# Kernel tuning notes

Hardware: AMD Instinct MI355X
Metric: run time of the kernel (lower is better)

Reference implementation:

```python
import jax, jax.numpy as jnp
import numpy as np

WS = 16        # window size
SHIFT = 8      # shift for odd blocks
DEPTH = 2      # number of stacked blocks
HEADS = 8
EPS = 1e-5


def window_partition(x, ws):
    # x: (B,H,W,C) -> (B*nw, ws*ws, C)
    B, H, W, C = x.shape
    x = x.reshape(B, H // ws, ws, W // ws, ws, C).transpose(0, 1, 3, 2, 4, 5)
    return x.reshape(-1, ws * ws, C)


def window_reverse(wins, ws, H, W):
    B = wins.shape[0] // ((H // ws) * (W // ws))
    x = wins.reshape(B, H // ws, W // ws, ws, ws, -1).transpose(0, 1, 3, 2, 4, 5)
    return x.reshape(B, H, W, -1)


def layernorm(x, g, b):
    m = jnp.mean(x, axis=-1, keepdims=True)
    v = jnp.mean(jnp.square(x - m), axis=-1, keepdims=True)
    return (x - m) * jax.lax.rsqrt(v + EPS) * g + b


def _make_rpi(ws):
    # Swin relative position index, shape (ws*ws, ws*ws), int32
    coords = np.stack(np.meshgrid(np.arange(ws), np.arange(ws), indexing='ij'))  # (2,ws,ws)
    coords = coords.reshape(2, -1)
    rel = coords[:, :, None] - coords[:, None, :]  # (2, n, n)
    rel = rel + (ws - 1)
    rpi = rel[0] * (2 * ws - 1) + rel[1]
    return jnp.asarray(rpi, dtype=jnp.int32)


def _make_attn_mask(H, W, ws, shift):
    # Swin shifted-window mask, shape (nw, n, n) with 0 / -100
    img = np.zeros((1, H, W, 1), dtype=np.float32)
    cnt = 0
    slices = (slice(0, -ws), slice(-ws, -shift), slice(-shift, None))
    for hs in slices:
        for wsl in slices:
            img[:, hs, wsl, :] = cnt
            cnt += 1
    mw = window_partition(jnp.asarray(img), ws).reshape(-1, ws * ws)  # (nw, n)
    mask = mw[:, None, :] - mw[:, :, None]
    return jnp.where(mask != 0, jnp.float32(-100.0), jnp.float32(0.0))


def setup_inputs() -> dict:
    key = jax.random.key(0)
    ks = jax.random.split(key, 8)
    B, H, W, C = 8, 64, 64, 256
    hid = 4 * C
    d = DEPTH
    s = 0.02
    inp = {
        'x':      jax.random.normal(ks[0], (B, H, W, C), jnp.float32),
        'ln1_g':  jnp.ones((d, C), jnp.float32),
        'ln1_b':  jnp.zeros((d, C), jnp.float32),
        'qkv_w':  jax.random.normal(ks[1], (d, C, 3 * C), jnp.float32) * s,
        'qkv_b':  jnp.zeros((d, 3 * C), jnp.float32),
        'rpb':    jax.random.normal(ks[2], (d, (2 * WS - 1) ** 2, HEADS), jnp.float32) * s,
        'proj_w': jax.random.normal(ks[3], (d, C, C), jnp.float32) * s,
        'proj_b': jnp.zeros((d, C), jnp.float32),
        'ln2_g':  jnp.ones((d, C), jnp.float32),
        'ln2_b':  jnp.zeros((d, C), jnp.float32),
        'fc1_w':  jax.random.normal(ks[4], (d, C, hid), jnp.float32) * s,
        'fc1_b':  jnp.zeros((d, hid), jnp.float32),
        'fc2_w':  jax.random.normal(ks[5], (d, hid, C), jnp.float32) * s,
        'fc2_b':  jnp.zeros((d, C), jnp.float32),
        'attn_mask': _make_attn_mask(H, W, WS, SHIFT),
        'rpi':    _make_rpi(WS),
    }
    return inp


def _forward(x, ln1_g, ln1_b, qkv_w, qkv_b, rpb, proj_w, proj_b,
             ln2_g, ln2_b, fc1_w, fc1_b, fc2_w, fc2_b, attn_mask, rpi):
    B, H, W, C = x.shape
    n = WS * WS
    hd = C // HEADS
    scale = jnp.float32(hd) ** -0.5
    for i in range(DEPTH):
        shift = SHIFT if (i % 2 == 1) else 0
        shortcut = x
        y = layernorm(x, ln1_g[i], ln1_b[i])
        if shift:
            y = jnp.roll(y, (-shift, -shift), axis=(1, 2))
        wins = window_partition(y, WS)                      # (b_, n, C)
        b_ = wins.shape[0]
        qkv = wins @ qkv_w[i] + qkv_b[i]
        qkv = qkv.reshape(b_, n, 3, HEADS, hd).transpose(2, 0, 3, 1, 4)
        q, k, v = qkv[0] * scale, qkv[1], qkv[2]            # (b_,h,n,hd)
        attn = jnp.einsum('bhnd,bhmd->bhnm', q, k)          # (b_,h,n,n)
        bias = rpb[i][rpi.reshape(-1)].reshape(n, n, HEADS).transpose(2, 0, 1)
        attn = attn + bias[None]
        if shift:
            nw = attn_mask.shape[0]
            attn = attn.reshape(B, nw, HEADS, n, n) + attn_mask[None, :, None]
            attn = attn.reshape(b_, HEADS, n, n)
        attn = jax.nn.softmax(attn, axis=-1)
        out = jnp.einsum('bhnm,bhmd->bhnd', attn, v)
        out = out.transpose(0, 2, 1, 3).reshape(b_, n, C)
        out = out @ proj_w[i] + proj_b[i]
        y = window_reverse(out, WS, H, W)
        if shift:
            y = jnp.roll(y, (shift, shift), axis=(1, 2))
        x = shortcut + y
        z = layernorm(x, ln2_g[i], ln2_b[i])
        z = jax.nn.gelu(z @ fc1_w[i] + fc1_b[i], approximate=False)
        z = z @ fc2_w[i] + fc2_b[i]
        x = x + z
    return x


def reference(x, ln1_g, ln1_b, qkv_w, qkv_b, rpb, proj_w, proj_b,
              ln2_g, ln2_b, fc1_w, fc1_b, fc2_w, fc2_b, attn_mask, rpi):
    return _forward(x, ln1_g, ln1_b, qkv_w, qkv_b, rpb, proj_w, proj_b,
                    ln2_g, ln2_b, fc1_w, fc1_b, fc2_w, fc2_b, attn_mask, rpi)
```

## Files before the change

### kernel.cpp

```cpp
#include <hip/hip_runtime.h>

typedef unsigned short u16;
typedef __attribute__((ext_vector_type(8))) short short8;
typedef __attribute__((ext_vector_type(4))) float f32x4;

#define GLDS16(gp, sp) __builtin_amdgcn_global_load_lds( \
    (const __attribute__((address_space(1))) void*)(gp),  \
    (__attribute__((address_space(3))) void*)(sp), 16, 0, 0)

__device__ __forceinline__ u16 f2bf(float f) {
  union { float f; unsigned u; } x; x.f = f;
  unsigned r = (x.u + 0x7fffu + ((x.u >> 16) & 1u)) >> 16;
  return (u16)r;
}
__device__ __forceinline__ float bf2f(u16 v) {
  union { unsigned u; float f; } x; x.u = ((unsigned)v) << 16; return x.f;
}

__global__ __launch_bounds__(256) void wswizB(const float* __restrict__ W,
                                              u16* __restrict__ Wf, int K, int N) {
  int tid = blockIdx.x * 256 + threadIdx.x;
  int Kt = K >> 5, Nt = N >> 4;
  int per = Nt * Kt * 64;
  if (tid >= 2 * per) return;
  int l = tid >= per;
  int rem = tid - l * per;
  int nb = rem / (Kt * 64);
  int rem2 = rem - nb * Kt * 64;
  int ks = rem2 >> 6, lane = rem2 & 63;
  int n = nb * 16 + (lane & 15);
  u16 o[8];
  #pragma unroll
  for (int e = 0; e < 8; ++e) {
    int k = ks * 32 + ((lane >> 4) << 3) + e;
    o[e] = f2bf(W[((size_t)l * K + k) * N + n]);
  }
  *(uint4*)(Wf + ((size_t)tid << 3)) = *(uint4*)o;
}

__global__ __launch_bounds__(256) void wswiz1(const float* __restrict__ W,
                                              u16* __restrict__ Wf) {
  int tid = blockIdx.x * 256 + threadIdx.x;
  int lane = tid & 63, nt = (tid >> 6) & 7, ks = (tid >> 9) & 7,
      hc = (tid >> 12) & 7, l = tid >> 15;
  int n = hc * 128 + nt * 16 + (lane & 15);
  u16 o[8];
  #pragma unroll
  for (int e = 0; e < 8; ++e) {
    int k = ks * 32 + ((lane >> 4) << 3) + e;
    o[e] = f2bf(W[((size_t)l * 256 + k) * 1024 + n]);
  }
  *(uint4*)(Wf + ((size_t)tid << 3)) = *(uint4*)o;
}

__global__ __launch_bounds__(256) void wswiz2(const float* __restrict__ W,
                                              u16* __restrict__ Wf) {
  int tid = blockIdx.x * 256 + threadIdx.x;
  int lane = tid & 63, nt = (tid >> 6) & 15, ks = (tid >> 10) & 3,
      hc = (tid >> 12) & 7, l = tid >> 15;
  int n = nt * 16 + (lane & 15);
  u16 o[8];
  #pragma unroll
  for (int e = 0; e < 8; ++e) {
    int k = hc * 128 + ks * 32 + ((lane >> 4) << 3) + e;
    o[e] = f2bf(W[((size_t)l * 1024 + k) * 256 + n]);
  }
  *(uint4*)(Wf + ((size_t)tid << 3)) = *(uint4*)o;
}

__global__ __launch_bounds__(256) void bias_gb(const float* __restrict__ rpb,
                                               const int* __restrict__ rpi,
                                               u16* __restrict__ biasb) {
  int tid = blockIdx.x * 256 + threadIdx.x;
  if (tid >= 131072) return;
  int l = tid >> 16, cid = tid & 65535;
  int lane = cid & 63, k = (cid >> 6) & 7, mslot = (cid >> 9) & 15, h = cid >> 13;
  u16 o[8];
  #pragma unroll
  for (int e = 0; e < 8; ++e) {
    int nt = 2 * k + (e >> 2), r = e & 3;
    int i = mslot * 16 + ((lane >> 4) << 2) + r;
    int j = nt * 16 + (lane & 15);
    int idx = rpi[i * 256 + j];
    o[e] = f2bf(rpb[((size_t)l * 961 + idx) * 8 + h]);
  }
  *(uint4*)(biasb + ((size_t)tid << 3)) = *(uint4*)o;
}

__global__ __launch_bounds__(256) void ln_part(const float* __restrict__ x,
                                               const float* __restrict__ g,
                                               const float* __restrict__ b,
                                               u16* __restrict__ out, int shift) {
  int wv = threadIdx.x >> 6, lane = threadIdx.x & 63;
  int wtok = blockIdx.x * 4 + wv;
  int w = wtok >> 8, t = wtok & 255;
  int bimg = w >> 4, wi = w & 15;
  int ph = (((wi >> 2) << 4) + (t >> 4) + shift) & 63;
  int pw = (((wi & 3) << 4) + (t & 15) + shift) & 63;
  const float4 v = *(const float4*)(x + ((size_t)((bimg * 64 + ph) * 64 + pw)) * 256 + lane * 4);
  float s = v.x + v.y + v.z + v.w;
  float sq = v.x * v.x + v.y * v.y + v.z * v.z + v.w * v.w;
  #pragma unroll
  for (int m = 1; m < 64; m <<= 1) { s += __shfl_xor(s, m, 64); sq += __shfl_xor(sq, m, 64); }
  float mean = s * (1.f / 256.f);
  float var = sq * (1.f / 256.f) - mean * mean;
  float rs = rsqrtf(var + 1e-5f);
  float4 gg = *(const float4*)(g + lane * 4);
  float4 bb = *(const float4*)(b + lane * 4);
  u16 o0 = f2bf((v.x - mean) * rs * gg.x + bb.x);
  u16 o1 = f2bf((v.y - mean) * rs * gg.y + bb.y);
  u16 o2 = f2bf((v.z - mean) * rs * gg.z + bb.z);
  u16 o3 = f2bf((v.w - mean) * rs * gg.w + bb.w);
  uint2 pk; pk.x = (unsigned)o0 | ((unsigned)o1 << 16); pk.y = (unsigned)o2 | ((unsigned)o3 << 16);
  *(uint2*)(out + (size_t)wtok * 256 + lane * 4) = pk;
}

struct EpiParams {
  const float* bias;
  u16* obf;
  float* of32;
  const float* resid;
  int shift;
  float qscale;
};

template <int EPI>
__global__ __launch_bounds__(512, 2) void gemm_fk(const u16* __restrict__ A,
                                                  const u16* __restrict__ Wf,
                                                  int N, EpiParams ep) {
  __shared__ u16 As[8][128][32];
  int tid = threadIdx.x;
  int n0 = blockIdx.x * 128, m0 = blockIdx.y * 128;
  int wv = tid >> 6, lane = tid & 63, quad = lane >> 4, l15 = lane & 15;
  int wm = wv & 1, wn = wv >> 1;

  #pragma unroll
  for (int i = 0; i < 8; ++i) {
    int c = i * 512 + tid;
    int kb = c >> 9, rc = c & 511;
    int row = rc >> 2, kc = (rc & 3) * 8;
    GLDS16(A + (size_t)(m0 + row) * 256 + kb * 32 + kc, &As[kb][row][kc]);
  }
  __syncthreads();

  f32x4 acc[4][2] = {};
  #pragma unroll
  for (int kb = 0; kb < 8; ++kb) {
    short8 bf[2];
    #pragma unroll
    for (int nt = 0; nt < 2; ++nt) {
      size_t ntile = (size_t)(blockIdx.x * 8 + wn * 2 + nt);
      bf[nt] = *(const short8*)(Wf + ((ntile * 8 + kb) * 64 + lane) * 8);
    }
    #pragma unroll
    for (int mt = 0; mt < 4; ++mt) {
      short8 af = *(const short8*)&As[kb][wm * 64 + mt * 16 + l15][quad * 8];
      #pragma unroll
      for (int nt = 0; nt < 2; ++nt)
        acc[mt][nt] = __builtin_amdgcn_mfma_f32_16x16x32_bf16(af, bf[nt], acc[mt][nt], 0, 0, 0);
    }
  }

  #pragma unroll
  for (int mt = 0; mt < 4; ++mt) {
    #pragma unroll
    for (int nt = 0; nt < 2; ++nt) {
      #pragma unroll
      for (int r = 0; r < 4; ++r) {
        int grow = m0 + wm * 64 + mt * 16 + quad * 4 + r;
        int gcol = n0 + wn * 32 + nt * 16 + l15;
        float v = acc[mt][nt][r] + ep.bias[gcol];
        if constexpr (EPI == 0) {
          if (gcol < 256) v *= ep.qscale;
          ep.obf[(size_t)grow * N + gcol] = f2bf(v);
        } else {
          int w_ = grow >> 8, t = grow & 255, wi = w_ & 15;
          int ph = (((wi >> 2) << 4) + (t >> 4) + ep.shift) & 63;
          int pw = (((wi & 3) << 4) + (t & 15) + ep.shift) & 63;
          size_t pix = (size_t)(((w_ >> 4) * 64 + ph) * 64 + pw);
          ep.of32[pix * 256 + gcol] = ep.resid[pix * 256 + gcol] + v;
        }
      }
    }
  }
}

__global__ __launch_bounds__(512, 4) void fused_mlp(const float* __restrict__ xin,
                                                    const float* __restrict__ g,
                                                    const float* __restrict__ b,
                                                    const u16* __restrict__ W1f,
                                                    const u16* __restrict__ W2f,
                                                    const float* __restrict__ b1p,
                                                    const float* __restrict__ b2p,
                                                    float* __restrict__ out) {
  __shared__ u16 Zs[64 * 264];
  __shared__ u16 Hs[2][64 * 136];
  int tid = threadIdx.x, wv = tid >> 6, lane = tid & 63;
  int quad = lane >> 4, l15 = lane & 15;
  int m0 = blockIdx.x * 64;

  float4 gg = *(const float4*)(g + lane * 4);
  float4 bb = *(const float4*)(b + lane * 4);
  #pragma unroll
  for (int rr = 0; rr < 8; ++rr) {
    int row = wv * 8 + rr;
    const float4 v = *(const float4*)(xin + (size_t)(m0 + row) * 256 + lane * 4);
    float s = v.x + v.y + v.z + v.w;
    float sq = v.x * v.x + v.y * v.y + v.z * v.z + v.w * v.w;
    #pragma unroll
    for (int m = 1; m < 64; m <<= 1) { s += __shfl_xor(s, m, 64); sq += __shfl_xor(sq, m, 64); }
    float mean = s * (1.f / 256.f);
    float var = sq * (1.f / 256.f) - mean * mean;
    float rs = rsqrtf(var + 1e-5f);
    u16 o0 = f2bf((v.x - mean) * rs * gg.x + bb.x);
    u16 o1 = f2bf((v.y - mean) * rs * gg.y + bb.y);
    u16 o2 = f2bf((v.z - mean) * rs * gg.z + bb.z);
    u16 o3 = f2bf((v.w - mean) * rs * gg.w + bb.w);
    uint2 pk; pk.x = (unsigned)o0 | ((unsigned)o1 << 16); pk.y = (unsigned)o2 | ((unsigned)o3 << 16);
    *(uint2*)&Zs[row * 264 + lane * 4] = pk;
  }
  __syncthreads();

  f32x4 acc2[4][2];
  #pragma unroll
  for (int nt = 0; nt < 2; ++nt) {
    float b2 = b2p[wv * 32 + nt * 16 + l15];
    #pragma unroll
    for (int mt = 0; mt < 4; ++mt)
      #pragma unroll
      for (int r = 0; r < 4; ++r) acc2[mt][nt][r] = b2;
  }

  for (int hc = 0; hc < 8; ++hc) {
    f32x4 acc1[4];
    {
      float b1 = b1p[hc * 128 + wv * 16 + l15];
      #pragma unroll
      for (int mt = 0; mt < 4; ++mt)
        #pragma unroll
        for (int r = 0; r < 4; ++r) acc1[mt][r] = b1;
    }
    #pragma unroll
    for (int ks = 0; ks < 8; ++ks) {
      short8 bf = *(const short8*)(W1f + ((((size_t)hc * 8 + ks) * 8 + wv) * 64 + lane) * 8);
      #pragma unroll
      for (int mt = 0; mt < 4; ++mt) {
        short8 af = *(const short8*)&Zs[(mt * 16 + l15) * 264 + ks * 32 + quad * 8];
        acc1[mt] = __builtin_amdgcn_mfma_f32_16x16x32_bf16(af, bf, acc1[mt], 0, 0, 0);
      }
    }
    u16* hs = &Hs[hc & 1][0];
    #pragma unroll
    for (int mt = 0; mt < 4; ++mt)
      #pragma unroll
      for (int r = 0; r < 4; ++r) {
        float v = acc1[mt][r];
        float inner = v * (1.f + 0.044715f * v * v);
        float e = __expf(-1.5957691216057308f * inner);
        float gl = v * __builtin_amdgcn_rcpf(1.f + e);
        hs[(mt * 16 + quad * 4 + r) * 136 + wv * 16 + l15] = f2bf(gl);
      }
    __syncthreads();
    #pragma unroll
    for (int ks = 0; ks < 4; ++ks) {
      short8 bf2[2];
      #pragma unroll
      for (int nt = 0; nt < 2; ++nt)
        bf2[nt] = *(const short8*)(W2f + ((((size_t)hc * 4 + ks) * 16 + wv * 2 + nt) * 64 + lane) * 8);
      #pragma unroll
      for (int mt = 0; mt < 4; ++mt) {
        short8 af2 = *(const short8*)&hs[(mt * 16 + l15) * 136 + ks * 32 + quad * 8];
        #pragma unroll
        for (int nt = 0; nt < 2; ++nt)
          acc2[mt][nt] = __builtin_amdgcn_mfma_f32_16x16x32_bf16(af2, bf2[nt], acc2[mt][nt], 0, 0, 0);
      }
    }
  }

  #pragma unroll
  for (int mt = 0; mt < 4; ++mt)
    #pragma unroll
    for (int nt = 0; nt < 2; ++nt)
      #pragma unroll
      for (int r = 0; r < 4; ++r) {
        size_t idx = (size_t)(m0 + mt * 16 + quad * 4 + r) * 256 + wv * 32 + nt * 16 + l15;
        out[idx] = xin[idx] + acc2[mt][nt][r];
      }
}

__global__ __launch_bounds__(256, 4) void attn_v3(const u16* __restrict__ qkv,
                                                  const u16* __restrict__ biasb,
                                                  int layer, u16* __restrict__ aout) {
  __shared__ u16 Klds[256 * 32];
  __shared__ u16 Vt[32 * 264];
  __shared__ u16 Plds[4][16 * 40];
  int bid = blockIdx.x;
  int lw = ((bid & 7) << 7) | (bid >> 3);
  int w = lw >> 3, h = lw & 7;
  int tid = threadIdx.x;

  {
    const uint4* kp = (const uint4*)(qkv + ((size_t)(w * 256 + tid)) * 768 + 256 + h * 32);
    uint4* kd = (uint4*)&Klds[tid * 32];
    kd[0] = kp[0]; kd[1] = kp[1]; kd[2] = kp[2]; kd[3] = kp[3];
    const uint4* vp = (const uint4*)(qkv + ((size_t)(w * 256 + tid)) * 768 + 512 + h * 32);
    u16 vt[32];
    *(uint4*)&vt[0]  = vp[0];
    *(uint4*)&vt[8]  = vp[1];
    *(uint4*)&vt[16] = vp[2];
    *(uint4*)&vt[24] = vp[3];
    #pragma unroll
    for (int d = 0; d < 32; ++d) Vt[d * 264 + tid] = vt[d];
  }
  __syncthreads();

  int wv = tid >> 6, lane = tid & 63, quad = lane >> 4, l15 = lane & 15;
  int wi = w & 15, wr = wi >> 2, wc = wi & 3;
  const bool masked = (layer != 0) && (wr == 3 || wc == 3);
  int rcj = (wc == 3) ? (l15 < 8 ? 1 : 2) : 0;

  #pragma unroll
  for (int mt = 0; mt < 4; ++mt) {
    int mslot = wv * 4 + mt;
    int m0 = mslot * 16;
    short8 aq = *(const short8*)(qkv + ((size_t)(w * 256 + m0 + l15)) * 768 + h * 32 + quad * 8);
    const u16* bmt = biasb + ((size_t)layer << 19) + ((size_t)h << 16) + (size_t)mslot * 4096;
    f32x4 c[16];
    #pragma unroll
    for (int k = 0; k < 8; ++k) {
      short8 bv = *(const short8*)(bmt + k * 512 + lane * 8);
      #pragma unroll
      for (int r = 0; r < 4; ++r) {
        c[2 * k][r]     = bf2f((u16)bv[r]);
        c[2 * k + 1][r] = bf2f((u16)bv[4 + r]);
      }
    }
    #pragma unroll
    for (int nt = 0; nt < 16; ++nt) {
      short8 bk = *(const short8*)&Klds[(nt * 16 + l15) * 32 + quad * 8];
      c[nt] = __builtin_amdgcn_mfma_f32_16x16x32_bf16(aq, bk, c[nt], 0, 0, 0);
    }
    if (masked) {
      int regi = ((wr == 3) ? (mslot < 8 ? 1 : 2) : 0) * 3 +
                 ((wc == 3) ? (quad < 2 ? 1 : 2) : 0);
      #pragma unroll
      for (int nt = 0; nt < 16; ++nt) {
        int regj = ((wr == 3) ? (nt < 8 ? 1 : 2) : 0) * 3 + rcj;
        float madd = (regi != regj) ? -100.f : 0.f;
        #pragma unroll
        for (int r = 0; r < 4; ++r) c[nt][r] += madd;
      }
    }
    float pm[4] = {-1e30f, -1e30f, -1e30f, -1e30f};
    #pragma unroll
    for (int nt = 0; nt < 16; ++nt)
      #pragma unroll
      for (int r = 0; r < 4; ++r) pm[r] = fmaxf(pm[r], c[nt][r]);
    #pragma unroll
    for (int r = 0; r < 4; ++r) {
      pm[r] = fmaxf(pm[r], __shfl_xor(pm[r], 1, 64));
      pm[r] = fmaxf(pm[r], __shfl_xor(pm[r], 2, 64));
      pm[r] = fmaxf(pm[r], __shfl_xor(pm[r], 4, 64));
      pm[r] = fmaxf(pm[r], __shfl_xor(pm[r], 8, 64));
    }
    float psum[4] = {0.f, 0.f, 0.f, 0.f};
    #pragma unroll
    for (int nt = 0; nt < 16; ++nt)
      #pragma unroll
      for (int r = 0; r < 4; ++r) {
        float e = __expf(c[nt][r] - pm[r]);
        c[nt][r] = e;
        psum[r] += e;
      }
    #pragma unroll
    for (int r = 0; r < 4; ++r) {
      psum[r] += __shfl_xor(psum[r], 1, 64);
      psum[r] += __shfl_xor(psum[r], 2, 64);
      psum[r] += __shfl_xor(psum[r], 4, 64);
      psum[r] += __shfl_xor(psum[r], 8, 64);
    }
    f32x4 o0 = {0.f, 0.f, 0.f, 0.f}, o1 = {0.f, 0.f, 0.f, 0.f};
    #pragma unroll
    for (int kk = 0; kk < 8; ++kk) {
      #pragma unroll
      for (int r = 0; r < 4; ++r) {
        Plds[wv][(quad * 4 + r) * 40 + l15] = f2bf(c[2 * kk][r]);
        Plds[wv][(quad * 4 + r) * 40 + 16 + l15] = f2bf(c[2 * kk + 1][r]);
      }
      short8 ap = *(const short8*)&Plds[wv][l15 * 40 + quad * 8];
      short8 bv0 = *(const short8*)&Vt[l15 * 264 + kk * 32 + quad * 8];
      short8 bv1 = *(const short8*)&Vt[(16 + l15) * 264 + kk * 32 + quad * 8];
      o0 = __builtin_amdgcn_mfma_f32_16x16x32_bf16(ap, bv0, o0, 0, 0, 0);
      o1 = __builtin_amdgcn_mfma_f32_16x16x32_bf16(ap, bv1, o1, 0, 0, 0);
    }
    #pragma unroll
    for (int r = 0; r < 4; ++r) {
      float inv = 1.f / psum[r];
      size_t row = (size_t)(w * 256 + m0 + quad * 4 + r);
      aout[row * 256 + h * 32 + l15] = f2bf(o0[r] * inv);
      aout[row * 256 + h * 32 + 16 + l15] = f2bf(o1[r] * inv);
    }
  }
}

extern "C" void kernel_launch(void* const* d_in, const int* in_sizes, int n_in,
                              void* d_out, int out_size, void* d_ws, size_t ws_size,
                              hipStream_t stream) {
  const float* x      = (const float*)d_in[0];
  const float* ln1_g  = (const float*)d_in[1];
  const float* ln1_b  = (const float*)d_in[2];
  const float* qkv_w  = (const float*)d_in[3];
  const float* qkv_b  = (const float*)d_in[4];
  const float* rpb    = (const float*)d_in[5];
  const float* proj_w = (const float*)d_in[6];
  const float* proj_b = (const float*)d_in[7];
  const float* ln2_g  = (const float*)d_in[8];
  const float* ln2_b  = (const float*)d_in[9];
  const float* fc1_w  = (const float*)d_in[10];
  const float* fc1_b  = (const float*)d_in[11];
  const float* fc2_w  = (const float*)d_in[12];
  const float* fc2_b  = (const float*)d_in[13];
  const int*   rpi    = (const int*)d_in[15];

  char* ws = (char*)d_ws;
  size_t off = 0;
  auto alloc = [&](size_t bytes) { void* p = ws + off; off += (bytes + 255) & ~(size_t)255; return p; };
  float* x_cur   = (float*)alloc((size_t)32768 * 256 * 4);
  u16* sbuf      = (u16*)alloc((size_t)32768 * 256 * 2);
  u16* qkvb      = (u16*)alloc((size_t)32768 * 768 * 2);
  u16* biasb     = (u16*)alloc((size_t)2 * 8 * 65536 * 2);
  u16* qkvF      = (u16*)alloc((size_t)2 * 196608 * 2);
  u16* projF     = (u16*)alloc((size_t)2 * 65536 * 2);
  u16* W1f       = (u16*)alloc((size_t)2 * 262144 * 2);
  u16* W2f       = (u16*)alloc((size_t)2 * 262144 * 2);

  wswizB<<<192, 256, 0, stream>>>(qkv_w, qkvF, 256, 768);
  wswizB<<<64, 256, 0, stream>>>(proj_w, projF, 256, 256);
  wswiz1<<<256, 256, 0, stream>>>(fc1_w, W1f);
  wswiz2<<<256, 256, 0, stream>>>(fc2_w, W2f);
  bias_gb<<<512, 256, 0, stream>>>(rpb, rpi, biasb);

  for (int i = 0; i < 2; ++i) {
    int shift = i ? 8 : 0;
    const float* xin = i ? x_cur : x;

    ln_part<<<8192, 256, 0, stream>>>(xin, ln1_g + i * 256, ln1_b + i * 256, sbuf, shift);

    EpiParams ep{};
    ep.bias = qkv_b + i * 768; ep.obf = qkvb; ep.qscale = 0.17677669529663687f;
    gemm_fk<0><<<dim3(6, 256), 512, 0, stream>>>(sbuf, qkvF + (size_t)i * 196608, 768, ep);

    attn_v3<<<1024, 256, 0, stream>>>(qkvb, biasb, i, sbuf);

    ep = EpiParams{};
    ep.bias = proj_b + i * 256; ep.of32 = x_cur; ep.resid = xin; ep.shift = shift;
    gemm_fk<2><<<dim3(2, 256), 512, 0, stream>>>(sbuf, projF + (size_t)i * 65536, 256, ep);

    fused_mlp<<<512, 512, 0, stream>>>(x_cur, ln2_g + i * 256, ln2_b + i * 256,
                                       W1f + (size_t)i * 262144, W2f + (size_t)i * 262144,
                                       fc1_b + i * 1024, fc2_b + i * 256,
                                       (i == 1) ? (float*)d_out : x_cur);
  }
}
```

Measured before the change: 423.6 us.

## Widen QKV GEMM tiles and process MLP hidden chunks in pairs

```diff
diff --git a/kernel.cpp b/kernel.cpp
--- a/kernel.cpp
+++ b/kernel.cpp
@@ -124,6 +124,58 @@
   float qscale;
 };
 
+__global__ __launch_bounds__(512, 2) void gemm_fk2(const u16* __restrict__ A,
+                                                   const u16* __restrict__ Wf,
+                                                   int N, EpiParams ep) {
+  __shared__ u16 As[8][128][32];
+  int tid = threadIdx.x;
+  int n0 = blockIdx.x * 256, m0 = blockIdx.y * 128;
+  int wv = tid >> 6, lane = tid & 63, quad = lane >> 4, l15 = lane & 15;
+  int wm = wv & 1, wn = wv >> 1;
+
+  #pragma unroll
+  for (int i = 0; i < 8; ++i) {
+    int c = i * 512 + tid;
+    int kb = c >> 9, rc = c & 511;
+    int row = rc >> 2, kc = (rc & 3) * 8;
+    GLDS16(A + (size_t)(m0 + row) * 256 + kb * 32 + kc, &As[kb][row][kc]);
+  }
+  __syncthreads();
+
+  f32x4 acc[4][4] = {};
+  #pragma unroll
+  for (int kb = 0; kb < 8; ++kb) {
+    short8 bf[4];
+    #pragma unroll
+    for (int nt = 0; nt < 4; ++nt) {
+      size_t ntile = (size_t)(blockIdx.x * 16 + wn * 4 + nt);
+      bf[nt] = *(const short8*)(Wf + ((ntile * 8 + kb) * 64 + lane) * 8);
+    }
+    #pragma unroll
+    for (int mt = 0; mt < 4; ++mt) {
+      short8 af = *(const short8*)&As[kb][wm * 64 + mt * 16 + l15][quad * 8];
+      #pragma unroll
+      for (int nt = 0; nt < 4; ++nt)
+        acc[mt][nt] = __builtin_amdgcn_mfma_f32_16x16x32_bf16(af, bf[nt], acc[mt][nt], 0, 0, 0);
+    }
+  }
+
+  #pragma unroll
+  for (int mt = 0; mt < 4; ++mt) {
+    #pragma unroll
+    for (int nt = 0; nt < 4; ++nt) {
+      #pragma unroll
+      for (int r = 0; r < 4; ++r) {
+        int grow = m0 + wm * 64 + mt * 16 + quad * 4 + r;
+        int gcol = n0 + wn * 64 + nt * 16 + l15;
+        float v = acc[mt][nt][r] + ep.bias[gcol];
+        if (gcol < 256) v *= ep.qscale;
+        ep.obf[(size_t)grow * N + gcol] = f2bf(v);
+      }
+    }
+  }
+}
+
 template <int EPI>
 __global__ __launch_bounds__(512, 2) void gemm_fk(const u16* __restrict__ A,
                                                   const u16* __restrict__ Wf,
@@ -231,50 +283,63 @@
       for (int r = 0; r < 4; ++r) acc2[mt][nt][r] = b2;
   }
 
-  for (int hc = 0; hc < 8; ++hc) {
-    f32x4 acc1[4];
+  for (int hp = 0; hp < 4; ++hp) {
+    int hcA = 2 * hp, hcB = 2 * hp + 1;
+    f32x4 acc1a[4], acc1b[4];
     {
-      float b1 = b1p[hc * 128 + wv * 16 + l15];
+      float b1a = b1p[hcA * 128 + wv * 16 + l15];
+      float b1b = b1p[hcB * 128 + wv * 16 + l15];
       #pragma unroll
       for (int mt = 0; mt < 4; ++mt)
         #pragma unroll
-        for (int r = 0; r < 4; ++r) acc1[mt][r] = b1;
+        for (int r = 0; r < 4; ++r) { acc1a[mt][r] = b1a; acc1b[mt][r] = b1b; }
     }
     #pragma unroll
     for (int ks = 0; ks < 8; ++ks) {
-      short8 bf = *(const short8*)(W1f + ((((size_t)hc * 8 + ks) * 8 + wv) * 64 + lane) * 8);
+      short8 bfa = *(const short8*)(W1f + ((((size_t)hcA * 8 + ks) * 8 + wv) * 64 + lane) * 8);
+      short8 bfb = *(const short8*)(W1f + ((((size_t)hcB * 8 + ks) * 8 + wv) * 64 + lane) * 8);
       #pragma unroll
       for (int mt = 0; mt < 4; ++mt) {
         short8 af = *(const short8*)&Zs[(mt * 16 + l15) * 264 + ks * 32 + quad * 8];
-        acc1[mt] = __builtin_amdgcn_mfma_f32_16x16x32_bf16(af, bf, acc1[mt], 0, 0, 0);
-      }
-    }
-    u16* hs = &Hs[hc & 1][0];
+        acc1a[mt] = __builtin_amdgcn_mfma_f32_16x16x32_bf16(af, bfa, acc1a[mt], 0, 0, 0);
+        acc1b[mt] = __builtin_amdgcn_mfma_f32_16x16x32_bf16(af, bfb, acc1b[mt], 0, 0, 0);
+      }
+    }
     #pragma unroll
     for (int mt = 0; mt < 4; ++mt)
       #pragma unroll
       for (int r = 0; r < 4; ++r) {
-        float v = acc1[mt][r];
-        float inner = v * (1.f + 0.044715f * v * v);
-        float e = __expf(-1.5957691216057308f * inner);
-        float gl = v * __builtin_amdgcn_rcpf(1.f + e);
-        hs[(mt * 16 + quad * 4 + r) * 136 + wv * 16 + l15] = f2bf(gl);
+        float va = acc1a[mt][r];
+        float ia = va * (1.f + 0.044715f * va * va);
+        float ea = __expf(-1.5957691216057308f * ia);
+        Hs[0][(mt * 16 + quad * 4 + r) * 136 + wv * 16 + l15] =
+            f2bf(va * __builtin_amdgcn_rcpf(1.f + ea));
+        float vb = acc1b[mt][r];
+        float ib = vb * (1.f + 0.044715f * vb * vb);
+        float eb = __expf(-1.5957691216057308f * ib);
+        Hs[1][(mt * 16 + quad * 4 + r) * 136 + wv * 16 + l15] =
+            f2bf(vb * __builtin_amdgcn_rcpf(1.f + eb));
       }
     __syncthreads();
     #pragma unroll
-    for (int ks = 0; ks < 4; ++ks) {
-      short8 bf2[2];
-      #pragma unroll
-      for (int nt = 0; nt < 2; ++nt)
-        bf2[nt] = *(const short8*)(W2f + ((((size_t)hc * 4 + ks) * 16 + wv * 2 + nt) * 64 + lane) * 8);
-      #pragma unroll
-      for (int mt = 0; mt < 4; ++mt) {
-        short8 af2 = *(const short8*)&hs[(mt * 16 + l15) * 136 + ks * 32 + quad * 8];
+    for (int buf = 0; buf < 2; ++buf) {
+      int hc = 2 * hp + buf;
+      #pragma unroll
+      for (int ks = 0; ks < 4; ++ks) {
+        short8 bf2[2];
         #pragma unroll
         for (int nt = 0; nt < 2; ++nt)
-          acc2[mt][nt] = __builtin_amdgcn_mfma_f32_16x16x32_bf16(af2, bf2[nt], acc2[mt][nt], 0, 0, 0);
-      }
-    }
+          bf2[nt] = *(const short8*)(W2f + ((((size_t)hc * 4 + ks) * 16 + wv * 2 + nt) * 64 + lane) * 8);
+        #pragma unroll
+        for (int mt = 0; mt < 4; ++mt) {
+          short8 af2 = *(const short8*)&Hs[buf][(mt * 16 + l15) * 136 + ks * 32 + quad * 8];
+          #pragma unroll
+          for (int nt = 0; nt < 2; ++nt)
+            acc2[mt][nt] = __builtin_amdgcn_mfma_f32_16x16x32_bf16(af2, bf2[nt], acc2[mt][nt], 0, 0, 0);
+        }
+      }
+    }
+    __syncthreads();
   }
 
   #pragma unroll
@@ -448,7 +513,7 @@
 
     EpiParams ep{};
     ep.bias = qkv_b + i * 768; ep.obf = qkvb; ep.qscale = 0.17677669529663687f;
-    gemm_fk<0><<<dim3(6, 256), 512, 0, stream>>>(sbuf, qkvF + (size_t)i * 196608, 768, ep);
+    gemm_fk2<<<dim3(3, 256), 512, 0, stream>>>(sbuf, qkvF + (size_t)i * 196608, 768, ep);
 
     attn_v3<<<1024, 256, 0, stream>>>(qkvb, biasb, i, sbuf);
 
```

New measurement: 405.2 us. 1.05x faster.
